# Optimization experiments

Measured on AMD Instinct MI355X. Metric: run time of the kernel, lower is better.

Reference implementation:

```python
import jax, jax.numpy as jnp
import numpy as np

N = 4096
D = 256
H = 8
HD = D // H
EPS = 1e-5
NEG = -1e9


def layer_norm(x, g, b):
    mu = jnp.mean(x, axis=-1, keepdims=True)
    var = jnp.mean(jnp.square(x - mu), axis=-1, keepdims=True)
    return (x - mu) * jax.lax.rsqrt(var + EPS) * g + b


def setup_inputs() -> dict:
    key = jax.random.key(0)
    ks = jax.random.split(key, 12)
    s = 1.0 / np.sqrt(D)
    inp = {
        "x": jax.random.normal(ks[0], (N, D), dtype=jnp.float32),
        "adj": jax.random.randint(ks[1], (N, N), 0, 2, dtype=jnp.int32),
        "Wq": jax.random.uniform(ks[2], (D, D), jnp.float32, -s, s),
        "Wk": jax.random.uniform(ks[3], (D, D), jnp.float32, -s, s),
        "Wv": jax.random.uniform(ks[4], (D, D), jnp.float32, -s, s),
        "bq": jnp.zeros((D,), jnp.float32),
        "bk": jnp.zeros((D,), jnp.float32),
        "bv": jnp.zeros((D,), jnp.float32),
        "Wo": jax.random.uniform(ks[5], (D, D), jnp.float32, -s, s),
        "bo": jnp.zeros((D,), jnp.float32),
        "g1": jnp.ones((D,), jnp.float32),
        "beta1": jnp.zeros((D,), jnp.float32),
        "W1": jax.random.uniform(ks[6], (2 * D, D), jnp.float32, -s, s),
        "b1": jnp.zeros((2 * D,), jnp.float32),
        "W2": jax.random.uniform(ks[7], (D, 2 * D), jnp.float32, -1.0 / np.sqrt(2 * D), 1.0 / np.sqrt(2 * D)),
        "b2": jnp.zeros((D,), jnp.float32),
        "g2": jnp.ones((D,), jnp.float32),
        "beta2": jnp.zeros((D,), jnp.float32),
    }
    return inp


def reference(x, adj, Wq, Wk, Wv, bq, bk, bv, Wo, bo, g1, beta1, W1, b1, W2, b2, g2, beta2):
    n = adj.shape[0]
    # allowed = adj + I > 0 ; attention only over neighbors + self-loop
    allowed = (adj + jnp.eye(n, dtype=adj.dtype)) > 0  # (n, n) bool

    q = (x @ Wq.T + bq).reshape(n, H, HD)
    k = (x @ Wk.T + bk).reshape(n, H, HD)
    v = (x @ Wv.T + bv).reshape(n, H, HD)

    scale = 1.0 / np.sqrt(HD)
    scores = jnp.einsum('nhd,mhd->hnm', q, k) * scale  # (H, n, n)
    scores = jnp.where(allowed[None, :, :], scores, NEG)
    attn = jax.nn.softmax(scores, axis=-1)
    o = jnp.einsum('hnm,mhd->nhd', attn, v).reshape(n, D)
    h = o @ Wo.T + bo

    x = layer_norm(x + h, g1, beta1)
    ffn = jax.nn.relu(x @ W1.T + b1) @ W2.T + b2
    x = layer_norm(x + ffn, g2, beta2)
    return x
```

## Files before the change

### kernel.cpp

```cpp
#include <hip/hip_runtime.h>
#include <hip/hip_bf16.h>

typedef __attribute__((ext_vector_type(4))) float f32x4;
typedef __attribute__((ext_vector_type(8))) short s16x8;

#define NROWS 4096
#define DMODEL 256
#define NHEAD 8
#define HDIM 32
#define PSTRIDE 72
#define OSTRIDE 33
#define M2C 24.0f
#define NM (NROWS * DMODEL)
#define SA_S 264
#define SH_S 268
#define SY_S 264
#define SR_S 520

__device__ __forceinline__ short bf16r(float f) {
    union { float f; unsigned u; } v; v.f = f;
    unsigned r = v.u + 0x7fffu + ((v.u >> 16) & 1u);
    return (short)(r >> 16);
}

__device__ __forceinline__ float fexp2(float x) {
    float r;
    asm("v_exp_f32 %0, %1" : "=v"(r) : "v"(x));
    return r;
}

__device__ __forceinline__ unsigned pk_bf16(float a, float b) {
#if __has_builtin(__builtin_amdgcn_cvt_pk_bf16_f32)
    typedef __bf16 bf2 __attribute__((ext_vector_type(2)));
    union { bf2 h; unsigned u; } c;
    c.h = __builtin_amdgcn_cvt_pk_bf16_f32(a, b);
    return c.u;
#else
    return (unsigned)(unsigned short)bf16r(a) | ((unsigned)(unsigned short)bf16r(b) << 16);
#endif
}

__device__ __forceinline__ s16x8 pack8(float4 a, float4 b) {
    s16x8 r;
    r[0] = bf16r(a.x); r[1] = bf16r(a.y); r[2] = bf16r(a.z); r[3] = bf16r(a.w);
    r[4] = bf16r(b.x); r[5] = bf16r(b.y); r[6] = bf16r(b.z); r[7] = bf16r(b.w);
    return r;
}

__global__ __launch_bounds__(256) void qkvprep_kernel(
        const float* __restrict__ X,
        const float* __restrict__ Wq, const float* __restrict__ Wk,
        const float* __restrict__ Wv,
        const float* __restrict__ bq, const float* __restrict__ bk,
        const float* __restrict__ bv,
        const int* __restrict__ adj, unsigned* __restrict__ mask,
        const float* __restrict__ Wo, const float* __restrict__ W1,
        const float* __restrict__ W2, short* __restrict__ Wb,
        short* __restrict__ Qb, short* __restrict__ Kb,
        short* __restrict__ Vtb) {
    const int b = blockIdx.x;
    const int tid = threadIdx.x;
    const int lane = tid & 63;
    if (b < 768) {
        const int wv = tid >> 6;
        const int quad = lane >> 4, col = lane & 15;
        const int bx = b & 63, by = b >> 6;
        const int o0 = by * 64;
        const int z = o0 >> 8;
        const float* Wsrc = (z == 0) ? Wq : (z == 1 ? Wk : Wv);
        const float* bias = (z == 0) ? bq : (z == 1 ? bk : bv);
        const int ow0 = o0 & 255;
        const int n0 = bx * 64 + wv * 16;
        const float QSC = 0.25505653437397888f;

        f32x4 zero = {0.f, 0.f, 0.f, 0.f};
        f32x4 acc[4] = {zero, zero, zero, zero};
        const float* ap = X + (size_t)(n0 + col) * DMODEL + quad * 8;
#pragma unroll
        for (int k0 = 0; k0 < DMODEL; k0 += 32) {
            float4 a0 = *(const float4*)(ap + k0);
            float4 a1 = *(const float4*)(ap + k0 + 4);
            s16x8 af = pack8(a0, a1);
#pragma unroll
            for (int t = 0; t < 4; ++t) {
                const float* wp = Wsrc + (size_t)(ow0 + t * 16 + col) * DMODEL + quad * 8 + k0;
                s16x8 bf = pack8(*(const float4*)wp, *(const float4*)(wp + 4));
                acc[t] = __builtin_amdgcn_mfma_f32_16x16x32_bf16(af, bf, acc[t], 0, 0, 0);
            }
        }
#pragma unroll
        for (int t = 0; t < 4; ++t) {
            const int oo = ow0 + t * 16 + col;
            float bvv = bias[oo];
#pragma unroll
            for (int r = 0; r < 4; ++r) {
                int n = n0 + quad * 4 + r;
                float v = acc[t][r] + bvv;
                if (z == 0)      Qb[(size_t)n * DMODEL + oo] = bf16r(v * QSC);
                else if (z == 1) Kb[(size_t)(oo >> 5) * NROWS * HDIM + (size_t)n * HDIM + (oo & 31)] = bf16r(v);
                else             Vtb[(size_t)oo * NROWS + n] = bf16r(v);
            }
        }
    } else if (b < 2816) {
        const int waveid = (b - 768) * 4 + (tid >> 6);
        int4 av[8];
        int rows[8], segs[8];
#pragma unroll
        for (int i = 0; i < 8; ++i) {
            const int task = waveid + i * 8192;
            rows[i] = task >> 4; segs[i] = task & 15;
            av[i] = *(const int4*)(adj + (size_t)rows[i] * NROWS + segs[i] * 256 + lane * 4);
        }
#pragma unroll
        for (int i = 0; i < 8; ++i) {
            const int row = rows[i];
            const int c0 = segs[i] * 256 + lane * 4;
            unsigned nib = (unsigned)(av[i].x > 0 || c0 == row)
                         | ((unsigned)(av[i].y > 0 || c0 + 1 == row) << 1)
                         | ((unsigned)(av[i].z > 0 || c0 + 2 == row) << 2)
                         | ((unsigned)(av[i].w > 0 || c0 + 3 == row) << 3);
            unsigned v = nib << ((lane & 7) * 4);
            v |= __shfl_xor((int)v, 1, 64);
            v |= __shfl_xor((int)v, 2, 64);
            v |= __shfl_xor((int)v, 4, 64);
            if ((lane & 7) == 0)
                mask[row * 128 + segs[i] * 8 + (lane >> 3)] = v;
        }
    } else {
        int i = (b - 2816) * 2048 + tid * 8;
        const float* src; int off;
        if (i < 65536)       { src = Wo; off = i; }
        else if (i < 196608) { src = W1; off = i - 65536; }
        else                 { src = W2; off = i - 196608; }
        float4 a = *(const float4*)(src + off);
        float4 c = *(const float4*)(src + off + 4);
        *(s16x8*)(Wb + i) = pack8(a, c);
    }
}

__global__ __launch_bounds__(256) void attn_kernel(const short* __restrict__ Qb,
                                                   const short* __restrict__ Kb,
                                                   const short* __restrict__ Vtb,
                                                   const unsigned* __restrict__ mask,
                                                   float* __restrict__ Opart,
                                                   float* __restrict__ lpart) {
    __shared__ union {
        short sP[2][16 * PSTRIDE];
        float sO[HDIM][OSTRIDE];
    } u[4];
    __shared__ float sl[4][32];

    const int tid = threadIdx.x;
    const int wv = tid >> 6, lane = tid & 63;
    const int quad = lane >> 4, col = lane & 15;
    const int khalf = blockIdx.x & 1;
    const int h = (blockIdx.x >> 1) & 7;
    const int q0 = (blockIdx.x >> 4) * 32;
    const int kw = khalf * 2048 + wv * 512;

    s16x8 qf[2];
    qf[0] = *(const s16x8*)(Qb + (size_t)(q0 + col) * DMODEL + h * HDIM + quad * 8);
    qf[1] = *(const s16x8*)(Qb + (size_t)(q0 + 16 + col) * DMODEL + h * HDIM + quad * 8);

    const short* kp  = Kb + (size_t)h * NROWS * HDIM + (size_t)(kw + col) * HDIM + quad * 8;
    const short* vp0 = Vtb + (size_t)(h * HDIM + col) * NROWS + kw + quad * 8;
    const short* vp1 = vp0 + (size_t)16 * NROWS;
    const unsigned* mp0 = mask + (size_t)(q0 + col) * 128 + (kw >> 5);
    const unsigned* mp1 = mp0 + 16 * 128;

    f32x4 zero = {0.f, 0.f, 0.f, 0.f};
    f32x4 acc[2][2] = {{zero, zero}, {zero, zero}};
    float rs[2] = {0.f, 0.f};
    const f32x4 cinit = {-M2C, -M2C, -M2C, -M2C};

#pragma unroll 1
    for (int it = 0; it < 8; ++it) {
        const short* k = kp + it * 64 * HDIM;
        s16x8 kf0 = *(const s16x8*)(k);
        s16x8 kf1 = *(const s16x8*)(k + 16 * HDIM);
        s16x8 kf2 = *(const s16x8*)(k + 32 * HDIM);
        s16x8 kf3 = *(const s16x8*)(k + 48 * HDIM);
        uint2 w0 = *(const uint2*)(mp0 + it * 2);
        uint2 w1 = *(const uint2*)(mp1 + it * 2);
        const short* v0 = vp0 + it * 64;
        const short* v1 = vp1 + it * 64;
        s16x8 vf00 = *(const s16x8*)(v0);
        s16x8 vf01 = *(const s16x8*)(v0 + 32);
        s16x8 vf10 = *(const s16x8*)(v1);
        s16x8 vf11 = *(const s16x8*)(v1 + 32);

#pragma unroll
        for (int qs = 0; qs < 2; ++qs) {
            unsigned wlo = (qs ? w1.x : w0.x) >> (quad * 4);
            unsigned whi = (qs ? w1.y : w0.y) >> (quad * 4);
            f32x4 st[4];
            st[0] = __builtin_amdgcn_mfma_f32_16x16x32_bf16(kf0, qf[qs], cinit, 0, 0, 0);
            st[1] = __builtin_amdgcn_mfma_f32_16x16x32_bf16(kf1, qf[qs], cinit, 0, 0, 0);
            st[2] = __builtin_amdgcn_mfma_f32_16x16x32_bf16(kf2, qf[qs], cinit, 0, 0, 0);
            st[3] = __builtin_amdgcn_mfma_f32_16x16x32_bf16(kf3, qf[qs], cinit, 0, 0, 0);

            float p[4][4];
            float r0 = 0.f;
#pragma unroll
            for (int t = 0; t < 4; ++t) {
                unsigned wm = (t < 2) ? wlo : whi;
#pragma unroll
                for (int r = 0; r < 4; ++r) {
                    float e = fexp2(st[t][r]);
                    bool ok = (wm & (1u << ((t & 1) * 16 + r))) != 0u;
                    p[t][r] = ok ? e : 0.f;
                    r0 += p[t][r];
                }
            }
            rs[qs] += r0;

            short* pb = &u[wv].sP[qs][0];
#pragma unroll
            for (int t = 0; t < 4; ++t) {
                uint2 pr;
                pr.x = pk_bf16(p[t][0], p[t][1]);
                pr.y = pk_bf16(p[t][2], p[t][3]);
                *(uint2*)(pb + col * PSTRIDE + t * 16 + quad * 4) = pr;
            }
            s16x8 pb0 = *(const s16x8*)(pb + col * PSTRIDE + quad * 8);
            s16x8 pb1 = *(const s16x8*)(pb + col * PSTRIDE + 32 + quad * 8);

            acc[qs][0] = __builtin_amdgcn_mfma_f32_16x16x32_bf16(vf00, pb0, acc[qs][0], 0, 0, 0);
            acc[qs][0] = __builtin_amdgcn_mfma_f32_16x16x32_bf16(vf01, pb1, acc[qs][0], 0, 0, 0);
            acc[qs][1] = __builtin_amdgcn_mfma_f32_16x16x32_bf16(vf10, pb0, acc[qs][1], 0, 0, 0);
            acc[qs][1] = __builtin_amdgcn_mfma_f32_16x16x32_bf16(vf11, pb1, acc[qs][1], 0, 0, 0);
        }
    }

#pragma unroll
    for (int qs = 0; qs < 2; ++qs) {
        float r = rs[qs];
        r += __shfl_xor(r, 16, 64);
        r += __shfl_xor(r, 32, 64);
        if (lane < 16) sl[wv][qs * 16 + col] = r;
#pragma unroll
        for (int rr = 0; rr < 4; ++rr) {
            u[wv].sO[quad * 4 + rr][qs * 16 + col]      = acc[qs][0][rr];
            u[wv].sO[16 + quad * 4 + rr][qs * 16 + col] = acc[qs][1][rr];
        }
    }
    __syncthreads();

    const int q = tid >> 3, hd0 = (tid & 7) * 4;
    float l = sl[0][q] + sl[1][q] + sl[2][q] + sl[3][q];
    float4 ov;
    ov.x = u[0].sO[hd0][q]     + u[1].sO[hd0][q]     + u[2].sO[hd0][q]     + u[3].sO[hd0][q];
    ov.y = u[0].sO[hd0 + 1][q] + u[1].sO[hd0 + 1][q] + u[2].sO[hd0 + 1][q] + u[3].sO[hd0 + 1][q];
    ov.z = u[0].sO[hd0 + 2][q] + u[1].sO[hd0 + 2][q] + u[2].sO[hd0 + 2][q] + u[3].sO[hd0 + 2][q];
    ov.w = u[0].sO[hd0 + 3][q] + u[1].sO[hd0 + 3][q] + u[2].sO[hd0 + 3][q] + u[3].sO[hd0 + 3][q];
    *(float4*)(Opart + (size_t)khalf * NM + (size_t)(q0 + q) * DMODEL + h * HDIM + hd0) = ov;
    if ((tid & 7) == 0) lpart[khalf * NROWS * NHEAD + (q0 + q) * NHEAD + h] = l;
}

__global__ __launch_bounds__(256) void mega_kernel(
        const float* __restrict__ Opart, const float* __restrict__ lpart,
        const float* __restrict__ X,
        const short* __restrict__ Wob, const short* __restrict__ W1b,
        const short* __restrict__ W2b,
        const float* __restrict__ bo,
        const float* __restrict__ g1, const float* __restrict__ be1,
        const float* __restrict__ b1, const float* __restrict__ b2,
        const float* __restrict__ g2, const float* __restrict__ be2,
        float* __restrict__ out) {
    __shared__ union { short sA[16 * SA_S]; short sR[16 * SR_S]; } uu;
    __shared__ float sH[16 * SH_S];
    __shared__ short sY[16 * SY_S];

    const int tid = threadIdx.x;
    const int wv = tid >> 6, lane = tid & 63;
    const int quad = lane >> 4, col = lane & 15;
    const int n0 = blockIdx.x * 16;
    const int rr_ = tid >> 4, cg = tid & 15;
    const int n_ln = n0 + rr_;
    f32x4 zero = {0.f, 0.f, 0.f, 0.f};

    {
        const int head = cg >> 1;
        float li = 1.f / (lpart[(size_t)n_ln * NHEAD + head] +
                          lpart[(size_t)NROWS * NHEAD + (size_t)n_ln * NHEAD + head]);
        const float* p0 = Opart + (size_t)n_ln * DMODEL + cg * 16;
        const float* p1 = p0 + NM;
        short* dst = &uu.sA[rr_ * SA_S + cg * 16];
#pragma unroll
        for (int j = 0; j < 4; ++j) {
            float4 a = ((const float4*)p0)[j];
            float4 b = ((const float4*)p1)[j];
            uint2 w;
            w.x = pk_bf16((a.x + b.x) * li, (a.y + b.y) * li);
            w.y = pk_bf16((a.z + b.z) * li, (a.w + b.w) * li);
            *(uint2*)(dst + j * 4) = w;
        }
    }
    __syncthreads();

    {
        const int o0 = wv * 64;
        f32x4 acc[4] = {zero, zero, zero, zero};
#pragma unroll
        for (int k0 = 0; k0 < DMODEL; k0 += 32) {
            s16x8 af = *(const s16x8*)&uu.sA[col * SA_S + k0 + quad * 8];
#pragma unroll
            for (int t = 0; t < 4; ++t) {
                s16x8 bf = *(const s16x8*)(Wob + (size_t)(o0 + t * 16 + col) * DMODEL + k0 + quad * 8);
                acc[t] = __builtin_amdgcn_mfma_f32_16x16x32_bf16(af, bf, acc[t], 0, 0, 0);
            }
        }
#pragma unroll
        for (int t = 0; t < 4; ++t) {
            int o = o0 + t * 16 + col;
            float bv = bo[o];
#pragma unroll
            for (int r = 0; r < 4; ++r)
                sH[(quad * 4 + r) * SH_S + o] = acc[t][r] + bv;
        }
    }
    __syncthreads();

    float y1v[16];
    {
        const float* xp = X + (size_t)n_ln * DMODEL + cg * 16;
        float v[16];
        float s = 0.f;
#pragma unroll
        for (int j = 0; j < 4; ++j) {
            float4 xv = ((const float4*)xp)[j];
            float4 hv = *(const float4*)&sH[rr_ * SH_S + cg * 16 + j * 4];
            v[j * 4 + 0] = xv.x + hv.x; v[j * 4 + 1] = xv.y + hv.y;
            v[j * 4 + 2] = xv.z + hv.z; v[j * 4 + 3] = xv.w + hv.w;
            s += v[j * 4] + v[j * 4 + 1] + v[j * 4 + 2] + v[j * 4 + 3];
        }
#pragma unroll
        for (int m = 1; m < 16; m <<= 1) s += __shfl_xor(s, m, 64);
        float mean = s * (1.f / 256.f);
        float q = 0.f;
#pragma unroll
        for (int i = 0; i < 16; ++i) { v[i] -= mean; q += v[i] * v[i]; }
#pragma unroll
        for (int m = 1; m < 16; m <<= 1) q += __shfl_xor(q, m, 64);
        float rstd = rsqrtf(q * (1.f / 256.f) + 1e-5f);
        const float* gp = g1 + cg * 16;
        const float* bp = be1 + cg * 16;
        short* dst = &sY[rr_ * SY_S + cg * 16];
#pragma unroll
        for (int j = 0; j < 4; ++j) {
            float4 gv = ((const float4*)gp)[j];
            float4 bev = ((const float4*)bp)[j];
            float a0 = v[j * 4 + 0] * rstd * gv.x + bev.x;
            float a1 = v[j * 4 + 1] * rstd * gv.y + bev.y;
            float a2 = v[j * 4 + 2] * rstd * gv.z + bev.z;
            float a3 = v[j * 4 + 3] * rstd * gv.w + bev.w;
            y1v[j * 4 + 0] = a0; y1v[j * 4 + 1] = a1;
            y1v[j * 4 + 2] = a2; y1v[j * 4 + 3] = a3;
            uint2 w;
            w.x = pk_bf16(a0, a1);
            w.y = pk_bf16(a2, a3);
            *(uint2*)(dst + j * 4) = w;
        }
    }
    __syncthreads();

    {
        const int o0 = wv * 128;
        f32x4 acc[8] = {zero, zero, zero, zero, zero, zero, zero, zero};
#pragma unroll
        for (int k0 = 0; k0 < DMODEL; k0 += 32) {
            s16x8 af = *(const s16x8*)&sY[col * SY_S + k0 + quad * 8];
#pragma unroll
            for (int t = 0; t < 8; ++t) {
                s16x8 bf = *(const s16x8*)(W1b + (size_t)(o0 + t * 16 + col) * DMODEL + k0 + quad * 8);
                acc[t] = __builtin_amdgcn_mfma_f32_16x16x32_bf16(af, bf, acc[t], 0, 0, 0);
            }
        }
#pragma unroll
        for (int t = 0; t < 8; ++t) {
            int o = o0 + t * 16 + col;
            float bv = b1[o];
#pragma unroll
            for (int r = 0; r < 4; ++r)
                uu.sR[(quad * 4 + r) * SR_S + o] = bf16r(fmaxf(acc[t][r] + bv, 0.f));
        }
    }
    __syncthreads();

    {
        const int o0 = wv * 64;
        f32x4 acc[4] = {zero, zero, zero, zero};
#pragma unroll
        for (int k0 = 0; k0 < 512; k0 += 32) {
            s16x8 af = *(const s16x8*)&uu.sR[col * SR_S + k0 + quad * 8];
#pragma unroll
            for (int t = 0; t < 4; ++t) {
                s16x8 bf = *(const s16x8*)(W2b + (size_t)(o0 + t * 16 + col) * 512 + k0 + quad * 8);
                acc[t] = __builtin_amdgcn_mfma_f32_16x16x32_bf16(af, bf, acc[t], 0, 0, 0);
            }
        }
#pragma unroll
        for (int t = 0; t < 4; ++t) {
            int o = o0 + t * 16 + col;
            float bv = b2[o];
#pragma unroll
            for (int r = 0; r < 4; ++r)
                sH[(quad * 4 + r) * SH_S + o] = acc[t][r] + bv;
        }
    }
    __syncthreads();

    {
        float v[16];
        float s = 0.f;
#pragma unroll
        for (int j = 0; j < 4; ++j) {
            float4 hv = *(const float4*)&sH[rr_ * SH_S + cg * 16 + j * 4];
            v[j * 4 + 0] = y1v[j * 4 + 0] + hv.x; v[j * 4 + 1] = y1v[j * 4 + 1] + hv.y;
            v[j * 4 + 2] = y1v[j * 4 + 2] + hv.z; v[j * 4 + 3] = y1v[j * 4 + 3] + hv.w;
            s += v[j * 4] + v[j * 4 + 1] + v[j * 4 + 2] + v[j * 4 + 3];
        }
#pragma unroll
        for (int m = 1; m < 16; m <<= 1) s += __shfl_xor(s, m, 64);
        float mean = s * (1.f / 256.f);
        float q = 0.f;
#pragma unroll
        for (int i = 0; i < 16; ++i) { v[i] -= mean; q += v[i] * v[i]; }
#pragma unroll
        for (int m = 1; m < 16; m <<= 1) q += __shfl_xor(q, m, 64);
        float rstd = rsqrtf(q * (1.f / 256.f) + 1e-5f);
        const float* gp = g2 + cg * 16;
        const float* bp = be2 + cg * 16;
        float* op = out + (size_t)n_ln * DMODEL + cg * 16;
#pragma unroll
        for (int j = 0; j < 4; ++j) {
            float4 gv = ((const float4*)gp)[j];
            float4 bev = ((const float4*)bp)[j];
            float4 y;
            y.x = v[j * 4 + 0] * rstd * gv.x + bev.x;
            y.y = v[j * 4 + 1] * rstd * gv.y + bev.y;
            y.z = v[j * 4 + 2] * rstd * gv.z + bev.z;
            y.w = v[j * 4 + 3] * rstd * gv.w + bev.w;
            ((float4*)op)[j] = y;
        }
    }
}

extern "C" void kernel_launch(void* const* d_in, const int* in_sizes, int n_in,
                              void* d_out, int out_size, void* d_ws, size_t ws_size,
                              hipStream_t stream) {
    const float* x   = (const float*)d_in[0];
    const int*   adj = (const int*)d_in[1];
    const float* Wq  = (const float*)d_in[2];
    const float* Wk  = (const float*)d_in[3];
    const float* Wv  = (const float*)d_in[4];
    const float* bq  = (const float*)d_in[5];
    const float* bk  = (const float*)d_in[6];
    const float* bv  = (const float*)d_in[7];
    const float* Wo  = (const float*)d_in[8];
    const float* bo  = (const float*)d_in[9];
    const float* g1  = (const float*)d_in[10];
    const float* be1 = (const float*)d_in[11];
    const float* W1  = (const float*)d_in[12];
    const float* b1  = (const float*)d_in[13];
    const float* W2  = (const float*)d_in[14];
    const float* b2  = (const float*)d_in[15];
    const float* g2  = (const float*)d_in[16];
    const float* be2 = (const float*)d_in[17];
    float* out = (float*)d_out;

    char* p = (char*)d_ws;
    unsigned* mask = (unsigned*)p; p += (size_t)NROWS * 128 * 4;
    short* Wb    = (short*)p;      p += (size_t)327680 * 2;
    short* Qb    = (short*)p;      p += (size_t)NM * 2;
    short* Kb    = (short*)p;      p += (size_t)NM * 2;
    short* Vtb   = (short*)p;      p += (size_t)NM * 2;
    float* Opart = (float*)p;      p += (size_t)2 * NM * 4;
    float* lpart = (float*)p;      p += (size_t)2 * NROWS * NHEAD * 4;

    qkvprep_kernel<<<dim3(2976), dim3(256), 0, stream>>>(
        x, Wq, Wk, Wv, bq, bk, bv, adj, mask, Wo, W1, W2, Wb, Qb, Kb, Vtb);
    attn_kernel<<<dim3(2048), dim3(256), 0, stream>>>(Qb, Kb, Vtb, mask, Opart, lpart);
    mega_kernel<<<dim3(256), dim3(256), 0, stream>>>(
        Opart, lpart, x, Wb, Wb + 65536, Wb + 196608,
        bo, g1, be1, b1, b2, g2, be2, out);
}
```

Baseline: 237.5 us.

## Stage V transpose through LDS and compute softmax row sums with MFMA

```diff
diff --git a/kernel.cpp b/kernel.cpp
--- a/kernel.cpp
+++ b/kernel.cpp
@@ -58,6 +58,7 @@
         const float* __restrict__ W2, short* __restrict__ Wb,
         short* __restrict__ Qb, short* __restrict__ Kb,
         short* __restrict__ Vtb) {
+    __shared__ short sT[64 * 72];
     const int b = blockIdx.x;
     const int tid = threadIdx.x;
     const int lane = tid & 63;
@@ -88,18 +89,37 @@
                 acc[t] = __builtin_amdgcn_mfma_f32_16x16x32_bf16(af, bf, acc[t], 0, 0, 0);
             }
         }
-#pragma unroll
-        for (int t = 0; t < 4; ++t) {
-            const int oo = ow0 + t * 16 + col;
-            float bvv = bias[oo];
-#pragma unroll
-            for (int r = 0; r < 4; ++r) {
-                int n = n0 + quad * 4 + r;
-                float v = acc[t][r] + bvv;
-                if (z == 0)      Qb[(size_t)n * DMODEL + oo] = bf16r(v * QSC);
-                else if (z == 1) Kb[(size_t)(oo >> 5) * NROWS * HDIM + (size_t)n * HDIM + (oo & 31)] = bf16r(v);
-                else             Vtb[(size_t)oo * NROWS + n] = bf16r(v);
-            }
+        if (z != 2) {
+#pragma unroll
+            for (int t = 0; t < 4; ++t) {
+                const int oo = ow0 + t * 16 + col;
+                float bvv = bias[oo];
+#pragma unroll
+                for (int r = 0; r < 4; ++r) {
+                    int n = n0 + quad * 4 + r;
+                    float v = acc[t][r] + bvv;
+                    if (z == 0) Qb[(size_t)n * DMODEL + oo] = bf16r(v * QSC);
+                    else        Kb[(size_t)(oo >> 5) * NROWS * HDIM + (size_t)n * HDIM + (oo & 31)] = bf16r(v);
+                }
+            }
+        } else {
+#pragma unroll
+            for (int t = 0; t < 4; ++t) {
+                const int oot = t * 16 + col;
+                float bvv = bias[ow0 + oot];
+#pragma unroll
+                for (int r = 0; r < 4; ++r) {
+                    int nn = wv * 16 + quad * 4 + r;
+                    sT[oot * 72 + nn] = bf16r(acc[t][r] + bvv);
+                }
+            }
+            __syncthreads();
+            const int oor = tid >> 2, nseg = (tid & 3) * 16;
+            s16x8 v0 = *(const s16x8*)&sT[oor * 72 + nseg];
+            s16x8 v1 = *(const s16x8*)&sT[oor * 72 + nseg + 8];
+            short* dst = Vtb + (size_t)(ow0 + oor) * NROWS + bx * 64 + nseg;
+            *(s16x8*)dst = v0;
+            *(s16x8*)(dst + 8) = v1;
         }
     } else if (b < 2816) {
         const int waveid = (b - 768) * 4 + (tid >> 6);
@@ -168,12 +188,15 @@
     const unsigned* mp0 = mask + (size_t)(q0 + col) * 128 + (kw >> 5);
     const unsigned* mp1 = mp0 + 16 * 128;
 
+    const short onev = (col == 0) ? (short)0x3F80 : (short)0;
+    const s16x8 ones = {onev, onev, onev, onev, onev, onev, onev, onev};
+
     f32x4 zero = {0.f, 0.f, 0.f, 0.f};
     f32x4 acc[2][2] = {{zero, zero}, {zero, zero}};
-    float rs[2] = {0.f, 0.f};
+    f32x4 lacc[2] = {zero, zero};
     const f32x4 cinit = {-M2C, -M2C, -M2C, -M2C};
 
-#pragma unroll 1
+#pragma unroll 2
     for (int it = 0; it < 8; ++it) {
         const short* k = kp + it * 64 * HDIM;
         s16x8 kf0 = *(const s16x8*)(k);
@@ -200,7 +223,6 @@
             st[3] = __builtin_amdgcn_mfma_f32_16x16x32_bf16(kf3, qf[qs], cinit, 0, 0, 0);
 
             float p[4][4];
-            float r0 = 0.f;
 #pragma unroll
             for (int t = 0; t < 4; ++t) {
                 unsigned wm = (t < 2) ? wlo : whi;
@@ -209,10 +231,8 @@
                     float e = fexp2(st[t][r]);
                     bool ok = (wm & (1u << ((t & 1) * 16 + r))) != 0u;
                     p[t][r] = ok ? e : 0.f;
-                    r0 += p[t][r];
                 }
             }
-            rs[qs] += r0;
 
             short* pb = &u[wv].sP[qs][0];
 #pragma unroll
@@ -229,15 +249,14 @@
             acc[qs][0] = __builtin_amdgcn_mfma_f32_16x16x32_bf16(vf01, pb1, acc[qs][0], 0, 0, 0);
             acc[qs][1] = __builtin_amdgcn_mfma_f32_16x16x32_bf16(vf10, pb0, acc[qs][1], 0, 0, 0);
             acc[qs][1] = __builtin_amdgcn_mfma_f32_16x16x32_bf16(vf11, pb1, acc[qs][1], 0, 0, 0);
+            lacc[qs] = __builtin_amdgcn_mfma_f32_16x16x32_bf16(ones, pb0, lacc[qs], 0, 0, 0);
+            lacc[qs] = __builtin_amdgcn_mfma_f32_16x16x32_bf16(ones, pb1, lacc[qs], 0, 0, 0);
         }
     }
 
 #pragma unroll
     for (int qs = 0; qs < 2; ++qs) {
-        float r = rs[qs];
-        r += __shfl_xor(r, 16, 64);
-        r += __shfl_xor(r, 32, 64);
-        if (lane < 16) sl[wv][qs * 16 + col] = r;
+        if (lane < 16) sl[wv][qs * 16 + col] = lacc[qs][0];
 #pragma unroll
         for (int rr = 0; rr < 4; ++rr) {
             u[wv].sO[quad * 4 + rr][qs * 16 + col]      = acc[qs][0][rr];
```

Measured after the change: 233.4 us. No clear change (-1.7%).
